# Performance work log

Hardware: AMD Instinct MI355X
Metric: run time of the kernel (lower is better)

Reference implementation:

```python
import jax, jax.numpy as jnp
import numpy as np
import math

V, D = 100000, 128
B, L = 4096, 200
INIT_MU = 0.1
INIT_RHO = math.log(math.exp(0.01 ** 0.5) - 1.0)  # softplus^-1(sqrt(init_sigma2))


def setup_inputs() -> dict:
    key = jax.random.key(0)
    k_mu, k_eps, k_x = jax.random.split(key, 3)
    W_mu = jax.random.uniform(k_mu, (V, D), jnp.float32, -INIT_MU, INIT_MU)
    W_rho = jnp.full((V, D), INIT_RHO, dtype=jnp.float32)
    eps = jax.random.normal(k_eps, (V, D), jnp.float32)
    x = jax.random.randint(k_x, (B, L), 0, V)
    return {"x": x, "W_mu": W_mu, "W_rho": W_rho, "eps": eps}


def reference(x, W_mu, W_rho, eps):
    # sigma = softplus(rho); sampled table = mu + sigma * clip(eps, -10, 10)
    W_sigma = jnp.log1p(jnp.exp(W_rho))
    sampled = W_mu + W_sigma * jnp.clip(eps, -10.0, 10.0)  # [V, D]
    return jnp.take(sampled, x, axis=0)  # [B, L, D]
```

## Files before the change

### kernel.cpp

```cpp
#include <hip/hip_runtime.h>
#include <hip/hip_bf16.h>

typedef float f32x4 __attribute__((ext_vector_type(4)));
typedef unsigned short u16;
typedef unsigned int   u32;
typedef u16 u16x4 __attribute__((ext_vector_type(4)));
typedef u16 u16x8 __attribute__((ext_vector_type(8)));

#define D4 32

__device__ __forceinline__ float softplus_f(float r) {
    return (r > 20.0f) ? r : log1pf(__expf(r));
}
__device__ __forceinline__ float clip10(float e) {
    return fminf(fmaxf(e, -10.0f), 10.0f);
}
__device__ __forceinline__ u16 f32_to_bf16_rne(float f) {
    u32 b = __float_as_uint(f);
    b += 0x7FFFu + ((b >> 16) & 1u);
    return (u16)(b >> 16);
}
__device__ __forceinline__ float bf16_to_f32(u16 h) {
    return __uint_as_float(((u32)h) << 16);
}

__global__ __launch_bounds__(256) void sample_table_bf16_kernel(
    const f32x4* __restrict__ mu,
    const f32x4* __restrict__ rho,
    const f32x4* __restrict__ eps,
    u16x4* __restrict__ tab,
    long n4)
{
    long t  = (long)blockIdx.x * blockDim.x + threadIdx.x;
    long j0 = t * 2, j1 = j0 + 1;
    if (j0 >= n4) return;

    f32x4 m0 = __builtin_nontemporal_load(&mu[j0]);
    f32x4 r0 = __builtin_nontemporal_load(&rho[j0]);
    f32x4 e0 = __builtin_nontemporal_load(&eps[j0]);

    u16x4 o0;
    o0.x = f32_to_bf16_rne(m0.x + softplus_f(r0.x) * clip10(e0.x));
    o0.y = f32_to_bf16_rne(m0.y + softplus_f(r0.y) * clip10(e0.y));
    o0.z = f32_to_bf16_rne(m0.z + softplus_f(r0.z) * clip10(e0.z));
    o0.w = f32_to_bf16_rne(m0.w + softplus_f(r0.w) * clip10(e0.w));

    if (j1 < n4) {
        f32x4 m1 = __builtin_nontemporal_load(&mu[j1]);
        f32x4 r1 = __builtin_nontemporal_load(&rho[j1]);
        f32x4 e1 = __builtin_nontemporal_load(&eps[j1]);
        u16x8 o;
        o[0] = o0.x; o[1] = o0.y; o[2] = o0.z; o[3] = o0.w;
        o[4] = f32_to_bf16_rne(m1.x + softplus_f(r1.x) * clip10(e1.x));
        o[5] = f32_to_bf16_rne(m1.y + softplus_f(r1.y) * clip10(e1.y));
        o[6] = f32_to_bf16_rne(m1.z + softplus_f(r1.z) * clip10(e1.z));
        o[7] = f32_to_bf16_rne(m1.w + softplus_f(r1.w) * clip10(e1.w));
        *(u16x8*)&tab[j0] = o;
    } else {
        tab[j0] = o0;
    }
}

__global__ __launch_bounds__(256) void gather_bf16_kernel(
    const int* __restrict__ x,
    const u16x4* __restrict__ tab,
    f32x4* __restrict__ out,
    int n_rows, int S)
{
    int g    = blockIdx.x * blockDim.x + threadIdx.x;
    int slot = g >> 5;
    int lane = g & 31;
    if (slot >= S) return;

    int r0 = slot, r1 = slot + S;
    bool h1 = (r1 < n_rows);
    int v0 = x[r0];
    int v1 = h1 ? x[r1] : v0;

    u16x4 a = tab[(long)v0 * D4 + lane];
    u16x4 b = tab[(long)v1 * D4 + lane];

    f32x4 A;
    A.x = bf16_to_f32(a.x); A.y = bf16_to_f32(a.y);
    A.z = bf16_to_f32(a.z); A.w = bf16_to_f32(a.w);
    __builtin_nontemporal_store(A, &out[(long)r0 * D4 + lane]);

    if (h1) {
        f32x4 B;
        B.x = bf16_to_f32(b.x); B.y = bf16_to_f32(b.y);
        B.z = bf16_to_f32(b.z); B.w = bf16_to_f32(b.w);
        __builtin_nontemporal_store(B, &out[(long)r1 * D4 + lane]);
    }
}

__global__ __launch_bounds__(256) void fused_kernel(
    const int* __restrict__ x,
    const f32x4* __restrict__ mu,
    const f32x4* __restrict__ rho,
    const f32x4* __restrict__ eps,
    f32x4* __restrict__ out,
    int n_rows)
{
    int tid  = blockIdx.x * blockDim.x + threadIdx.x;
    int row  = tid >> 5;
    int lane = tid & 31;
    if (row >= n_rows) return;
    long src = (long)x[row] * D4 + lane;
    f32x4 m = mu[src], r = rho[src], e = eps[src];
    f32x4 o;
    o.x = m.x + softplus_f(r.x) * clip10(e.x);
    o.y = m.y + softplus_f(r.y) * clip10(e.y);
    o.z = m.z + softplus_f(r.z) * clip10(e.z);
    o.w = m.w + softplus_f(r.w) * clip10(e.w);
    out[(long)row * D4 + lane] = o;
}

extern "C" void kernel_launch(void* const* d_in, const int* in_sizes, int n_in,
                              void* d_out, int out_size, void* d_ws, size_t ws_size,
                              hipStream_t stream)
{
    const int*   x   = (const int*)  d_in[0];
    const f32x4* mu  = (const f32x4*)d_in[1];
    const f32x4* rho = (const f32x4*)d_in[2];
    const f32x4* eps = (const f32x4*)d_in[3];
    f32x4* out = (f32x4*)d_out;

    int  n_rows      = in_sizes[0];
    long table_elems = (long)in_sizes[1];
    size_t table_bytes_bf16 = (size_t)table_elems * sizeof(u16);
    const int block = 256;

    if (ws_size >= table_bytes_bf16) {
        u16x4* tab = (u16x4*)d_ws;
        long n4 = table_elems / 4;

        long threads1 = (n4 + 1) / 2;
        int grid1 = (int)((threads1 + block - 1) / block);
        sample_table_bf16_kernel<<<grid1, block, 0, stream>>>(mu, rho, eps, tab, n4);

        int S = (n_rows + 1) / 2;
        long threads2 = (long)S * 32;
        int grid2 = (int)((threads2 + block - 1) / block);
        gather_bf16_kernel<<<grid2, block, 0, stream>>>(x, tab, out, n_rows, S);
    } else {
        long threads = (long)n_rows * 32;
        int grid = (int)((threads + block - 1) / block);
        fused_kernel<<<grid, block, 0, stream>>>(x, mu, rho, eps, out, n_rows);
    }
}
```

Baseline: 147.2 us.

## Partition gather by vocabulary slice per XCD to keep table rows in local L2

The gather kernel now assigns each block a vocabulary slice chosen by blockIdx modulo 8. Round-robin block dispatch across XCDs means each XCD only reads table rows from its own slice, so that slice can stay resident in its L2. Each wave ballots over 64 indices and serially copies the matching rows, one 64-lane load and store per row. Every index is read by all 8 buckets, and the per-row loop with narrower stores may lower memory-level parallelism. Softplus also switches from log1pf to the fast __logf(1+exp) form, which is less accurate.

```diff
diff --git a/kernel.cpp b/kernel.cpp
--- a/kernel.cpp
+++ b/kernel.cpp
@@ -1,16 +1,18 @@
 #include <hip/hip_runtime.h>
 #include <hip/hip_bf16.h>
 
+typedef float f32x2 __attribute__((ext_vector_type(2)));
 typedef float f32x4 __attribute__((ext_vector_type(4)));
 typedef unsigned short u16;
 typedef unsigned int   u32;
 typedef u16 u16x4 __attribute__((ext_vector_type(4)));
 typedef u16 u16x8 __attribute__((ext_vector_type(8)));
 
-#define D4 32
+#define D4  32
+#define NXCD 8
 
 __device__ __forceinline__ float softplus_f(float r) {
-    return (r > 20.0f) ? r : log1pf(__expf(r));
+    return (r > 20.0f) ? r : __logf(1.0f + __expf(r));
 }
 __device__ __forceinline__ float clip10(float e) {
     return fminf(fmaxf(e, -10.0f), 10.0f);
@@ -61,35 +63,40 @@
     }
 }
 
-__global__ __launch_bounds__(256) void gather_bf16_kernel(
+__global__ __launch_bounds__(256) void gather_sliced_kernel(
     const int* __restrict__ x,
-    const u16x4* __restrict__ tab,
-    f32x4* __restrict__ out,
-    int n_rows, int S)
+    const u32* __restrict__ tab,
+    f32x2* __restrict__ out,
+    int n_rows, int vslice, int chunk)
 {
-    int g    = blockIdx.x * blockDim.x + threadIdx.x;
-    int slot = g >> 5;
-    int lane = g & 31;
-    if (slot >= S) return;
+    int bucket  = blockIdx.x & (NXCD - 1);
+    int chunkid = blockIdx.x >> 3;
+    int lo = bucket * vslice;
+    int hi = lo + vslice;
 
-    int r0 = slot, r1 = slot + S;
-    bool h1 = (r1 < n_rows);
-    int v0 = x[r0];
-    int v1 = h1 ? x[r1] : v0;
+    long base = (long)chunkid * chunk;
+    long end  = base + chunk;
+    if (end > n_rows) end = n_rows;
 
-    u16x4 a = tab[(long)v0 * D4 + lane];
-    u16x4 b = tab[(long)v1 * D4 + lane];
+    int wid  = threadIdx.x >> 6;
+    int lane = threadIdx.x & 63;
 
-    f32x4 A;
-    A.x = bf16_to_f32(a.x); A.y = bf16_to_f32(a.y);
-    A.z = bf16_to_f32(a.z); A.w = bf16_to_f32(a.w);
-    __builtin_nontemporal_store(A, &out[(long)r0 * D4 + lane]);
-
-    if (h1) {
-        f32x4 B;
-        B.x = bf16_to_f32(b.x); B.y = bf16_to_f32(b.y);
-        B.z = bf16_to_f32(b.z); B.w = bf16_to_f32(b.w);
-        __builtin_nontemporal_store(B, &out[(long)r1 * D4 + lane]);
+    for (long r = base + (long)wid * 64; r < end; r += 256) {
+        long rr = r + lane;
+        int  v  = (rr < end) ? x[rr] : -1;
+        bool mine = (v >= lo) & (v < hi);
+        unsigned long long mask = __ballot(mine);
+        while (mask) {
+            int bit = __ffsll((long long)mask) - 1;
+            mask &= mask - 1;
+            int  vv   = __shfl(v, bit);
+            long orow = r + bit;
+            u32 w = tab[(long)vv * 64 + lane];
+            f32x2 f;
+            f.x = bf16_to_f32((u16)(w & 0xffffu));
+            f.y = bf16_to_f32((u16)(w >> 16));
+            __builtin_nontemporal_store(f, &out[orow * 64 + lane]);
+        }
     }
 }
 
@@ -123,28 +130,30 @@
     const f32x4* mu  = (const f32x4*)d_in[1];
     const f32x4* rho = (const f32x4*)d_in[2];
     const f32x4* eps = (const f32x4*)d_in[3];
-    f32x4* out = (f32x4*)d_out;
 
     int  n_rows      = in_sizes[0];
     long table_elems = (long)in_sizes[1];
+    int  V           = (int)(table_elems / 128);
     size_t table_bytes_bf16 = (size_t)table_elems * sizeof(u16);
     const int block = 256;
 
     if (ws_size >= table_bytes_bf16) {
-        u16x4* tab = (u16x4*)d_ws;
         long n4 = table_elems / 4;
 
         long threads1 = (n4 + 1) / 2;
         int grid1 = (int)((threads1 + block - 1) / block);
-        sample_table_bf16_kernel<<<grid1, block, 0, stream>>>(mu, rho, eps, tab, n4);
+        sample_table_bf16_kernel<<<grid1, block, 0, stream>>>(
+            mu, rho, eps, (u16x4*)d_ws, n4);
 
-        int S = (n_rows + 1) / 2;
-        long threads2 = (long)S * 32;
-        int grid2 = (int)((threads2 + block - 1) / block);
-        gather_bf16_kernel<<<grid2, block, 0, stream>>>(x, tab, out, n_rows, S);
+        int vslice = (V + NXCD - 1) / NXCD;
+        int chunk  = 1024;
+        int nchunks = (n_rows + chunk - 1) / chunk;
+        int grid2 = nchunks * NXCD;
+        gather_sliced_kernel<<<grid2, block, 0, stream>>>(
+            x, (const u32*)d_ws, (f32x2*)d_out, n_rows, vslice, chunk);
     } else {
         long threads = (long)n_rows * 32;
         int grid = (int)((threads + block - 1) / block);
-        fused_kernel<<<grid, block, 0, stream>>>(x, mu, rho, eps, out, n_rows);
+        fused_kernel<<<grid, block, 0, stream>>>(x, mu, rho, eps, (f32x4*)d_out, n_rows);
     }
 }
```

Result: faster. 139.3 us (median of 2 runs) (-5.3%).
